# Optimization experiments

Hardware: AMD Instinct MI355X
Metric: run time of the kernel (lower is better)

Reference implementation:

```python
import jax, jax.numpy as jnp
import numpy as np
import math

NEG = -10000.0

def setup_inputs() -> dict:
    key = jax.random.key(0)
    kq, kk, kv, km = jax.random.split(key, 4)
    B, H, S, D = 4, 16, 2048, 64
    q = jax.random.normal(kq, (B, H, S, D), dtype=jnp.float32)
    k = jax.random.normal(kk, (B, H, S, D), dtype=jnp.float32)
    v = jax.random.normal(kv, (B, H, S, D), dtype=jnp.float32)
    mask = jax.random.randint(km, (B, 1, 1, S), 0, 2, dtype=jnp.int32)
    return {"q": q, "k": k, "v": v, "mask": mask}

def reference(q, k, v, mask):
    # scores: [B,H,S,S]
    scale = 1.0 / math.sqrt(q.shape[-1])
    x = jnp.einsum('bhqd,bhkd->bhqk', q, k) * scale
    x = x + mask.astype(x.dtype) * jnp.asarray(NEG, x.dtype)
    p = jax.nn.softmax(x, axis=-1)
    # dropout is identity in eval mode
    return jnp.einsum('bhqk,bhkd->bhqd', p, v)
```

## Files before the change

kernel.cpp:

```cpp
#include <hip/hip_runtime.h>

#define SQ 2048
#define DH 64
#define NH 16
#define NB 4
#define QBLK 64
#define KBLK 64
#define LOG2E 1.4426950408889634f
#define SHIFT 16.0f

#define WS_K_OFF  0
#define WS_V_OFF  16777216
#define WS_B_OFF  33554432
#define WS_NEED   (33554432 + 32768)

typedef __attribute__((ext_vector_type(8))) __bf16 bf16x8;
typedef __attribute__((ext_vector_type(4))) float f32x4;
typedef __attribute__((ext_vector_type(4))) unsigned int u32x4;

typedef bf16x8 __attribute__((may_alias)) bf16x8a;
typedef u32x4  __attribute__((may_alias)) u32x4a;
typedef unsigned int   __attribute__((may_alias)) u32a;
typedef unsigned short __attribute__((may_alias)) u16a;

union bfrag { bf16x8 v; __bf16 b[8]; unsigned short u[8]; u32x4 q4; };

__device__ __forceinline__ unsigned short bfbits(__bf16 x) {
    return __builtin_bit_cast(unsigned short, x);
}

__device__ __forceinline__ void gload16(const void* g, void* l) {
    __builtin_amdgcn_global_load_lds(
        (const __attribute__((address_space(1))) unsigned int*)g,
        (__attribute__((address_space(3))) unsigned int*)l, 16, 0, 0);
}


__global__ __launch_bounds__(256) void prep_k(const float* __restrict__ kin,
                                              char* __restrict__ kout) {
    int t8 = (blockIdx.x * 256 + threadIdx.x) * 8;
    f32x4 a = *(const f32x4*)(kin + t8);
    f32x4 b = *(const f32x4*)(kin + t8 + 4);
    bfrag c;
    #pragma unroll
    for (int j = 0; j < 4; ++j) { c.b[j] = (__bf16)a[j]; c.b[j+4] = (__bf16)b[j]; }
    *(u32x4a*)(kout + t8 * 2) = c.q4;
}

__global__ __launch_bounds__(256) void prep_v(const float* __restrict__ vin,
                                              char* __restrict__ vout) {
    __shared__ __align__(16) char vt[8192];
    const int tid = threadIdx.x;
    const int bh = blockIdx.y, kb = blockIdx.x;
    const float* vp = vin + (size_t)bh * SQ * DH + (size_t)(kb * 64 + (tid & 31) * 2) * DH + (tid >> 5) * 8;
    int k0 = (tid & 31) * 2, d0 = (tid >> 5) * 8;
    f32x4 a0 = *(const f32x4*)vp;
    f32x4 a1 = *(const f32x4*)(vp + 4);
    f32x4 b0 = *(const f32x4*)(vp + DH);
    f32x4 b1 = *(const f32x4*)(vp + DH + 4);
    #pragma unroll
    for (int j = 0; j < 4; ++j) {
        unsigned v1 = (unsigned)bfbits((__bf16)a0[j]) | ((unsigned)bfbits((__bf16)b0[j]) << 16);
        *(u32a*)(vt + (d0 + j) * 128 + k0 * 2) = v1;
        unsigned v2 = (unsigned)bfbits((__bf16)a1[j]) | ((unsigned)bfbits((__bf16)b1[j]) << 16);
        *(u32a*)(vt + (d0 + 4 + j) * 128 + k0 * 2) = v2;
    }
    __syncthreads();
    #pragma unroll
    for (int i = 0; i < 2; ++i) {
        int c = tid + i * 256;
        int row = c >> 3, col = (c & 7) * 16;
        u32x4 val = *(const u32x4a*)(vt + row * 128 + col);
        *(u32x4a*)(vout + (size_t)bh * 262144 + row * 4096 + kb * 128 + col) = val;
    }
}

__global__ __launch_bounds__(256) void prep_bias(const int* __restrict__ mask,
                                                 float* __restrict__ bias) {
    int i = blockIdx.x * 256 + threadIdx.x;
    bias[i] = (float)mask[i] * (-10000.0f * LOG2E) - SHIFT;
}


__global__ __launch_bounds__(256) void attn_fwd_main(
    const float* __restrict__ qg, const char* __restrict__ Kg,
    const char* __restrict__ Vg, const float* __restrict__ biasg,
    float* __restrict__ outg)
{
    __shared__ __align__(16) char smem[40960];

    const int tid  = threadIdx.x;
    const int w    = tid >> 6;
    const int lane = tid & 63;
    const int g    = lane >> 4;
    const int li   = lane & 15;

    const int qb = blockIdx.x;
    const int bh = blockIdx.y;
    const int bb = bh >> 4;
    const size_t hoff = (size_t)bh * SQ * DH;

    bfrag qf0, qf1;
    {
        const float* qp = qg + hoff + (size_t)(qb * QBLK + w * 16 + li) * DH + g * 8;
        f32x4 a = *(const f32x4*)qp;
        f32x4 b = *(const f32x4*)(qp + 4);
        f32x4 c = *(const f32x4*)(qp + 32);
        f32x4 d = *(const f32x4*)(qp + 36);
        #pragma unroll
        for (int j = 0; j < 4; ++j) {
            qf0.b[j]     = (__bf16)a[j];
            qf0.b[j + 4] = (__bf16)b[j];
            qf1.b[j]     = (__bf16)c[j];
            qf1.b[j + 4] = (__bf16)d[j];
        }
    }

    const int Lb0 = w * 2048 + lane * 16;
    const int Lb1 = Lb0 + 1024;
    const int srcK0 = Lb0 ^ (((Lb0 >> 7) & 7) << 4);
    const int srcK1 = Lb1 ^ (((Lb1 >> 7) & 7) << 4);
    const int rV0 = Lb0 >> 7, rV1 = Lb1 >> 7;
    const int srcV0 = rV0 * 4096 + ((Lb0 & 127) ^ ((rV0 & 7) << 4));
    const int srcV1 = rV1 * 4096 + ((Lb1 & 127) ^ ((rV1 & 7) << 4));

    const char* Kgb = Kg + ((size_t)bh << 18);
    const char* Vgb = Vg + ((size_t)bh << 18);
    const float* bgb = biasg + bb * SQ + li;

    float l_part[4] = {0.f, 0.f, 0.f, 0.f};
    const f32x4 z4 = {0.f, 0.f, 0.f, 0.f};
    f32x4 acc[4] = {z4, z4, z4, z4};
    const float kscale = 0.125f * LOG2E;

    {
        const char* kg = Kgb;             char* kl = smem + w * 2048;
        const char* vp = Vgb;             char* vl = smem + 16384 + w * 2048;
        gload16(kg + srcK0, kl);
        gload16(kg + srcK1, kl + 1024);
        gload16(vp + srcV0, vl);
        gload16(vp + srcV1, vl + 1024);
    }
    asm volatile("s_waitcnt vmcnt(0)" ::: "memory");
    __syncthreads();

    #pragma unroll 1
    for (int kt = 0; kt < SQ / KBLK; ++kt) {
        const int cur = kt & 1;
        if (kt < SQ / KBLK - 1) {
            const int nb = cur ^ 1;
            const char* kg = Kgb + ((kt + 1) << 13);  char* kl = smem + nb * 8192 + w * 2048;
            const char* vp = Vgb + ((kt + 1) << 7);   char* vl = smem + 16384 + nb * 8192 + w * 2048;
            gload16(kg + srcK0, kl);
            gload16(kg + srcK1, kl + 1024);
            gload16(vp + srcV0, vl);
            gload16(vp + srcV1, vl + 1024);
        }
        char* Ks = smem + cur * 8192;
        char* Vt = smem + 16384 + cur * 8192;

        const float* bp = bgb + kt * 64;
        float bt0 = bp[0], bt1 = bp[16], bt2 = bp[32], bt3 = bp[48];

        float p[4][4];
        #pragma unroll
        for (int t = 0; t < 4; ++t) {
            int key  = t * 16 + li;
            int kswz = (key & 7) << 4;
            bf16x8 kf0 = *(const bf16x8a*)(Ks + ((key * 128 + g * 16) ^ kswz));
            bf16x8 kf1 = *(const bf16x8a*)(Ks + ((key * 128 + 64 + g * 16) ^ kswz));
            f32x4 s4 = __builtin_amdgcn_mfma_f32_16x16x32_bf16(qf0.v, kf0, z4, 0, 0, 0);
            s4 = __builtin_amdgcn_mfma_f32_16x16x32_bf16(qf1.v, kf1, s4, 0, 0, 0);
            float bt = (t == 0) ? bt0 : (t == 1) ? bt1 : (t == 2) ? bt2 : bt3;
            #pragma unroll
            for (int r = 0; r < 4; ++r) p[t][r] = exp2f(s4[r] * kscale + bt);
        }
        #pragma unroll
        for (int r = 0; r < 4; ++r)
            l_part[r] += (p[0][r] + p[1][r]) + (p[2][r] + p[3][r]);

        char* Pw = smem + 32768 + (w << 11);
        #pragma unroll
        for (int t = 0; t < 4; ++t) {
            #pragma unroll
            for (int r = 0; r < 4; ++r) {
                int qr  = g * 4 + r;
                int off = qr * 128 + (t * 16 + li) * 2;
                *(u16a*)(Pw + (off ^ ((qr & 7) << 4))) = bfbits((__bf16)p[t][r]);
            }
        }
        int pswz = (li & 7) << 4;
        bf16x8 pf0 = *(const bf16x8a*)(Pw + ((li * 128 + g * 16) ^ pswz));
        bf16x8 pf1 = *(const bf16x8a*)(Pw + ((li * 128 + 64 + g * 16) ^ pswz));
        #pragma unroll
        for (int dt = 0; dt < 4; ++dt) {
            int d    = dt * 16 + li;
            int dswz = (d & 7) << 4;
            bf16x8 vf0 = *(const bf16x8a*)(Vt + ((d * 128 + g * 16) ^ dswz));
            bf16x8 vf1 = *(const bf16x8a*)(Vt + ((d * 128 + 64 + g * 16) ^ dswz));
            acc[dt] = __builtin_amdgcn_mfma_f32_16x16x32_bf16(pf0, vf0, acc[dt], 0, 0, 0);
            acc[dt] = __builtin_amdgcn_mfma_f32_16x16x32_bf16(pf1, vf1, acc[dt], 0, 0, 0);
        }

        asm volatile("s_waitcnt vmcnt(0)" ::: "memory");
        __syncthreads();
    }

    #pragma unroll
    for (int off = 1; off < 16; off <<= 1) {
        #pragma unroll
        for (int r = 0; r < 4; ++r)
            l_part[r] += __shfl_xor(l_part[r], off);
    }
    #pragma unroll
    for (int r = 0; r < 4; ++r) {
        float inv = 1.0f / l_part[r];
        float* op = outg + hoff + (size_t)(qb * QBLK + w * 16 + g * 4 + r) * DH + li;
        #pragma unroll
        for (int dt = 0; dt < 4; ++dt)
            op[dt * 16] = acc[dt][r] * inv;
    }
}


__global__ __launch_bounds__(256) void attn_fwd_fallback(
    const float* __restrict__ qg, const float* __restrict__ kg,
    const float* __restrict__ vg, const int* __restrict__ maskg,
    float* __restrict__ outg)
{
    __shared__ __align__(16) char smem[24832];
    char* Ks = smem;
    char* Vt = smem + 8192;
    char* Pb = smem + 16384;
    float* biass = (float*)(smem + 24576);

    const int tid  = threadIdx.x;
    const int w    = tid >> 6;
    const int lane = tid & 63;
    const int g    = lane >> 4;
    const int li   = lane & 15;

    const int qb = blockIdx.x;
    const int bh = blockIdx.y;
    const int bb = bh >> 4;
    const size_t hoff = (size_t)bh * SQ * DH;

    bfrag qf0, qf1;
    {
        const float* qp = qg + hoff + (size_t)(qb * QBLK + w * 16 + li) * DH + g * 8;
        f32x4 a = *(const f32x4*)qp;
        f32x4 b = *(const f32x4*)(qp + 4);
        f32x4 c = *(const f32x4*)(qp + 32);
        f32x4 d = *(const f32x4*)(qp + 36);
        #pragma unroll
        for (int j = 0; j < 4; ++j) {
            qf0.b[j]     = (__bf16)a[j];
            qf0.b[j + 4] = (__bf16)b[j];
            qf1.b[j]     = (__bf16)c[j];
            qf1.b[j + 4] = (__bf16)d[j];
        }
    }

    float l_part[4] = {0.f, 0.f, 0.f, 0.f};
    const f32x4 z4 = {0.f, 0.f, 0.f, 0.f};
    f32x4 acc[4] = {z4, z4, z4, z4};
    const float kscale = 0.125f * LOG2E;

    #pragma unroll 1
    for (int kt = 0; kt < SQ / KBLK; ++kt) {
        __syncthreads();
        {
            const float* kp = kg + hoff + (size_t)kt * (KBLK * DH) + tid * 16;
            f32x4 a0 = ((const f32x4*)kp)[0];
            f32x4 a1 = ((const f32x4*)kp)[1];
            f32x4 a2 = ((const f32x4*)kp)[2];
            f32x4 a3 = ((const f32x4*)kp)[3];
            bfrag c0, c1;
            #pragma unroll
            for (int j = 0; j < 4; ++j) {
                c0.b[j]     = (__bf16)a0[j];
                c0.b[j + 4] = (__bf16)a1[j];
                c1.b[j]     = (__bf16)a2[j];
                c1.b[j + 4] = (__bf16)a3[j];
            }
            int krow = tid >> 2;
            int base = krow * 128 + (tid & 3) * 32;
            int swz  = (krow & 7) << 4;
            *(u32x4a*)(Ks + ((base) ^ swz))      = c0.q4;
            *(u32x4a*)(Ks + ((base + 16) ^ swz)) = c1.q4;
        }
        {
            int k0 = (tid & 31) * 2;
            int d0 = (tid >> 5) * 8;
            const float* vp = vg + hoff + (size_t)(kt * KBLK + k0) * DH + d0;
            f32x4 a0 = *(const f32x4*)vp;
            f32x4 a1 = *(const f32x4*)(vp + 4);
            f32x4 b0 = *(const f32x4*)(vp + DH);
            f32x4 b1 = *(const f32x4*)(vp + DH + 4);
            #pragma unroll
            for (int j = 0; j < 4; ++j) {
                int d1 = d0 + j;
                unsigned v1 = (unsigned)bfbits((__bf16)a0[j]) | ((unsigned)bfbits((__bf16)b0[j]) << 16);
                *(u32a*)(Vt + ((d1 * 128 + k0 * 2) ^ ((d1 & 7) << 4))) = v1;
                int d2 = d0 + 4 + j;
                unsigned v2 = (unsigned)bfbits((__bf16)a1[j]) | ((unsigned)bfbits((__bf16)b1[j]) << 16);
                *(u32a*)(Vt + ((d2 * 128 + k0 * 2) ^ ((d2 & 7) << 4))) = v2;
            }
        }
        if (tid < KBLK) {
            biass[tid] = (float)maskg[bb * SQ + kt * KBLK + tid] * (-10000.0f * LOG2E) - SHIFT;
        }
        __syncthreads();

        float p[4][4];
        #pragma unroll
        for (int t = 0; t < 4; ++t) {
            int key  = t * 16 + li;
            int kswz = (key & 7) << 4;
            bf16x8 kf0 = *(const bf16x8a*)(Ks + ((key * 128 + g * 16) ^ kswz));
            bf16x8 kf1 = *(const bf16x8a*)(Ks + ((key * 128 + 64 + g * 16) ^ kswz));
            f32x4 s4 = __builtin_amdgcn_mfma_f32_16x16x32_bf16(qf0.v, kf0, z4, 0, 0, 0);
            s4 = __builtin_amdgcn_mfma_f32_16x16x32_bf16(qf1.v, kf1, s4, 0, 0, 0);
            float bt = biass[key];
            #pragma unroll
            for (int r = 0; r < 4; ++r) p[t][r] = exp2f(s4[r] * kscale + bt);
        }
        #pragma unroll
        for (int r = 0; r < 4; ++r)
            l_part[r] += (p[0][r] + p[1][r]) + (p[2][r] + p[3][r]);

        char* Pw = Pb + (w << 11);
        #pragma unroll
        for (int t = 0; t < 4; ++t) {
            #pragma unroll
            for (int r = 0; r < 4; ++r) {
                int qr  = g * 4 + r;
                int off = qr * 128 + (t * 16 + li) * 2;
                *(u16a*)(Pw + (off ^ ((qr & 7) << 4))) = bfbits((__bf16)p[t][r]);
            }
        }
        int pswz = (li & 7) << 4;
        bf16x8 pf0 = *(const bf16x8a*)(Pw + ((li * 128 + g * 16) ^ pswz));
        bf16x8 pf1 = *(const bf16x8a*)(Pw + ((li * 128 + 64 + g * 16) ^ pswz));
        #pragma unroll
        for (int dt = 0; dt < 4; ++dt) {
            int d    = dt * 16 + li;
            int dswz = (d & 7) << 4;
            bf16x8 vf0 = *(const bf16x8a*)(Vt + ((d * 128 + g * 16) ^ dswz));
            bf16x8 vf1 = *(const bf16x8a*)(Vt + ((d * 128 + 64 + g * 16) ^ dswz));
            acc[dt] = __builtin_amdgcn_mfma_f32_16x16x32_bf16(pf0, vf0, acc[dt], 0, 0, 0);
            acc[dt] = __builtin_amdgcn_mfma_f32_16x16x32_bf16(pf1, vf1, acc[dt], 0, 0, 0);
        }
    }

    #pragma unroll
    for (int off = 1; off < 16; off <<= 1) {
        #pragma unroll
        for (int r = 0; r < 4; ++r)
            l_part[r] += __shfl_xor(l_part[r], off);
    }
    #pragma unroll
    for (int r = 0; r < 4; ++r) {
        float inv = 1.0f / l_part[r];
        float* op = outg + hoff + (size_t)(qb * QBLK + w * 16 + g * 4 + r) * DH + li;
        #pragma unroll
        for (int dt = 0; dt < 4; ++dt)
            op[dt * 16] = acc[dt][r] * inv;
    }
}

extern "C" void kernel_launch(void* const* d_in, const int* in_sizes, int n_in,
                              void* d_out, int out_size, void* d_ws, size_t ws_size,
                              hipStream_t stream) {
    const float* q = (const float*)d_in[0];
    const float* k = (const float*)d_in[1];
    const float* v = (const float*)d_in[2];
    const int* mask = (const int*)d_in[3];
    float* out = (float*)d_out;
    dim3 grid(SQ / QBLK, NB * NH);
    if (ws_size >= (size_t)WS_NEED) {
        char* ws = (char*)d_ws;
        prep_k<<<4096, 256, 0, stream>>>(k, ws + WS_K_OFF);
        prep_v<<<dim3(32, 64), 256, 0, stream>>>(v, ws + WS_V_OFF);
        prep_bias<<<32, 256, 0, stream>>>(mask, (float*)(ws + WS_B_OFF));
        attn_fwd_main<<<grid, 256, 0, stream>>>(q, ws + WS_K_OFF, ws + WS_V_OFF,
                                                (const float*)(ws + WS_B_OFF), out);
    } else {
        attn_fwd_fallback<<<grid, 256, 0, stream>>>(q, k, v, mask, out);
    }
}
```

Measured before the change: 268.4 us.

## Double query tile to 128 with 512 threads and tile-contiguous V layout

```diff
diff --git a/kernel.cpp b/kernel.cpp
--- a/kernel.cpp
+++ b/kernel.cpp
@@ -4,7 +4,7 @@
 #define DH 64
 #define NH 16
 #define NB 4
-#define QBLK 64
+#define QBLK 128
 #define KBLK 64
 #define LOG2E 1.4426950408889634f
 #define SHIFT 16.0f
@@ -52,8 +52,8 @@
     __shared__ __align__(16) char vt[8192];
     const int tid = threadIdx.x;
     const int bh = blockIdx.y, kb = blockIdx.x;
-    const float* vp = vin + (size_t)bh * SQ * DH + (size_t)(kb * 64 + (tid & 31) * 2) * DH + (tid >> 5) * 8;
     int k0 = (tid & 31) * 2, d0 = (tid >> 5) * 8;
+    const float* vp = vin + (size_t)bh * SQ * DH + (size_t)(kb * 64 + k0) * DH + d0;
     f32x4 a0 = *(const f32x4*)vp;
     f32x4 a1 = *(const f32x4*)(vp + 4);
     f32x4 b0 = *(const f32x4*)(vp + DH);
@@ -66,12 +66,11 @@
         *(u32a*)(vt + (d0 + 4 + j) * 128 + k0 * 2) = v2;
     }
     __syncthreads();
+    char* outp = vout + ((size_t)bh << 18) + ((size_t)kb << 13);
     #pragma unroll
     for (int i = 0; i < 2; ++i) {
-        int c = tid + i * 256;
-        int row = c >> 3, col = (c & 7) * 16;
-        u32x4 val = *(const u32x4a*)(vt + row * 128 + col);
-        *(u32x4a*)(vout + (size_t)bh * 262144 + row * 4096 + kb * 128 + col) = val;
+        int c = (tid + i * 256) * 16;
+        *(u32x4a*)(outp + c) = *(const u32x4a*)(vt + c);
     }
 }
 
@@ -82,12 +81,12 @@
 }
 
 
-__global__ __launch_bounds__(256) void attn_fwd_main(
+__global__ __launch_bounds__(512) void attn_fwd_main(
     const float* __restrict__ qg, const char* __restrict__ Kg,
     const char* __restrict__ Vg, const float* __restrict__ biasg,
     float* __restrict__ outg)
 {
-    __shared__ __align__(16) char smem[40960];
+    __shared__ __align__(16) char smem[49152];
 
     const int tid  = threadIdx.x;
     const int w    = tid >> 6;
@@ -100,6 +99,7 @@
     const int bb = bh >> 4;
     const size_t hoff = (size_t)bh * SQ * DH;
 
+    const float kscale = 0.125f * LOG2E;
     bfrag qf0, qf1;
     {
         const float* qp = qg + hoff + (size_t)(qb * QBLK + w * 16 + li) * DH + g * 8;
@@ -109,20 +109,15 @@
         f32x4 d = *(const f32x4*)(qp + 36);
         #pragma unroll
         for (int j = 0; j < 4; ++j) {
-            qf0.b[j]     = (__bf16)a[j];
-            qf0.b[j + 4] = (__bf16)b[j];
-            qf1.b[j]     = (__bf16)c[j];
-            qf1.b[j + 4] = (__bf16)d[j];
-        }
-    }
-
-    const int Lb0 = w * 2048 + lane * 16;
-    const int Lb1 = Lb0 + 1024;
-    const int srcK0 = Lb0 ^ (((Lb0 >> 7) & 7) << 4);
-    const int srcK1 = Lb1 ^ (((Lb1 >> 7) & 7) << 4);
-    const int rV0 = Lb0 >> 7, rV1 = Lb1 >> 7;
-    const int srcV0 = rV0 * 4096 + ((Lb0 & 127) ^ ((rV0 & 7) << 4));
-    const int srcV1 = rV1 * 4096 + ((Lb1 & 127) ^ ((rV1 & 7) << 4));
+            qf0.b[j]     = (__bf16)(a[j] * kscale);
+            qf0.b[j + 4] = (__bf16)(b[j] * kscale);
+            qf1.b[j]     = (__bf16)(c[j] * kscale);
+            qf1.b[j + 4] = (__bf16)(d[j] * kscale);
+        }
+    }
+
+    const int L    = w * 1024 + lane * 16;
+    const int srcX = L ^ (((L >> 7) & 7) << 4);
 
     const char* Kgb = Kg + ((size_t)bh << 18);
     const char* Vgb = Vg + ((size_t)bh << 18);
@@ -131,16 +126,9 @@
     float l_part[4] = {0.f, 0.f, 0.f, 0.f};
     const f32x4 z4 = {0.f, 0.f, 0.f, 0.f};
     f32x4 acc[4] = {z4, z4, z4, z4};
-    const float kscale = 0.125f * LOG2E;
-
-    {
-        const char* kg = Kgb;             char* kl = smem + w * 2048;
-        const char* vp = Vgb;             char* vl = smem + 16384 + w * 2048;
-        gload16(kg + srcK0, kl);
-        gload16(kg + srcK1, kl + 1024);
-        gload16(vp + srcV0, vl);
-        gload16(vp + srcV1, vl + 1024);
-    }
+
+    gload16(Kgb + srcX, smem + L);
+    gload16(Vgb + srcX, smem + 16384 + L);
     asm volatile("s_waitcnt vmcnt(0)" ::: "memory");
     __syncthreads();
 
@@ -149,12 +137,8 @@
         const int cur = kt & 1;
         if (kt < SQ / KBLK - 1) {
             const int nb = cur ^ 1;
-            const char* kg = Kgb + ((kt + 1) << 13);  char* kl = smem + nb * 8192 + w * 2048;
-            const char* vp = Vgb + ((kt + 1) << 7);   char* vl = smem + 16384 + nb * 8192 + w * 2048;
-            gload16(kg + srcK0, kl);
-            gload16(kg + srcK1, kl + 1024);
-            gload16(vp + srcV0, vl);
-            gload16(vp + srcV1, vl + 1024);
+            gload16(Kgb + ((kt + 1) << 13) + srcX, smem + nb * 8192 + L);
+            gload16(Vgb + ((kt + 1) << 13) + srcX, smem + 16384 + nb * 8192 + L);
         }
         char* Ks = smem + cur * 8192;
         char* Vt = smem + 16384 + cur * 8192;
@@ -173,7 +157,7 @@
             s4 = __builtin_amdgcn_mfma_f32_16x16x32_bf16(qf1.v, kf1, s4, 0, 0, 0);
             float bt = (t == 0) ? bt0 : (t == 1) ? bt1 : (t == 2) ? bt2 : bt3;
             #pragma unroll
-            for (int r = 0; r < 4; ++r) p[t][r] = exp2f(s4[r] * kscale + bt);
+            for (int r = 0; r < 4; ++r) p[t][r] = exp2f(s4[r] + bt);
         }
         #pragma unroll
         for (int r = 0; r < 4; ++r)
@@ -247,7 +231,7 @@
 
     bfrag qf0, qf1;
     {
-        const float* qp = qg + hoff + (size_t)(qb * QBLK + w * 16 + li) * DH + g * 8;
+        const float* qp = qg + hoff + (size_t)(qb * 64 + w * 16 + li) * DH + g * 8;
         f32x4 a = *(const f32x4*)qp;
         f32x4 b = *(const f32x4*)(qp + 4);
         f32x4 c = *(const f32x4*)(qp + 32);
@@ -362,7 +346,7 @@
     #pragma unroll
     for (int r = 0; r < 4; ++r) {
         float inv = 1.0f / l_part[r];
-        float* op = outg + hoff + (size_t)(qb * QBLK + w * 16 + g * 4 + r) * DH + li;
+        float* op = outg + hoff + (size_t)(qb * 64 + w * 16 + g * 4 + r) * DH + li;
         #pragma unroll
         for (int dt = 0; dt < 4; ++dt)
             op[dt * 16] = acc[dt][r] * inv;
@@ -377,15 +361,16 @@
     const float* v = (const float*)d_in[2];
     const int* mask = (const int*)d_in[3];
     float* out = (float*)d_out;
-    dim3 grid(SQ / QBLK, NB * NH);
     if (ws_size >= (size_t)WS_NEED) {
         char* ws = (char*)d_ws;
         prep_k<<<4096, 256, 0, stream>>>(k, ws + WS_K_OFF);
         prep_v<<<dim3(32, 64), 256, 0, stream>>>(v, ws + WS_V_OFF);
         prep_bias<<<32, 256, 0, stream>>>(mask, (float*)(ws + WS_B_OFF));
-        attn_fwd_main<<<grid, 256, 0, stream>>>(q, ws + WS_K_OFF, ws + WS_V_OFF,
+        dim3 grid(SQ / QBLK, NB * NH);
+        attn_fwd_main<<<grid, 512, 0, stream>>>(q, ws + WS_K_OFF, ws + WS_V_OFF,
                                                 (const float*)(ws + WS_B_OFF), out);
     } else {
+        dim3 grid(SQ / 64, NB * NH);
         attn_fwd_fallback<<<grid, 256, 0, stream>>>(q, k, v, mask, out);
     }
 }
```

Result: faster. 254.6 us (-5.1%).
